# Performance work log

Measured on AMD Instinct MI355X. Metric: run time of the kernel, lower is better.

## Reference

```python
import jax, jax.numpy as jnp
import numpy as np

N = 100000
E = 1600000
NIN = 128
NOUT = 128


def setup_inputs() -> dict:
    key = jax.random.key(0)
    k1, k2, k3, k4 = jax.random.split(key, 4)
    x = jax.random.normal(k1, (N, NIN), dtype=jnp.float32)
    edge_index = jax.random.randint(k2, (2, E), 0, N, dtype=jnp.int64)
    edge_attr = jnp.ones((E,), dtype=jnp.float32)  # unused by GCNConv
    # PyG Linear weight is [out, in]; glorot-ish init
    W = jax.random.normal(k3, (NOUT, NIN), dtype=jnp.float32) / np.sqrt(NIN)
    b = jnp.zeros((NOUT,), dtype=jnp.float32)
    return {"x": x, "edge_index": edge_index, "edge_attr": edge_attr, "W": W, "b": b}


def reference(x, edge_index, edge_attr, W, b):
    # PyG GCNConv: add self-loops, symmetric degree normalization,
    # linear transform, scatter-add aggregation at destination, + bias.
    n = x.shape[0]
    loops = jnp.arange(n, dtype=edge_index.dtype)
    src = jnp.concatenate([edge_index[0], loops])  # [E+N]
    dst = jnp.concatenate([edge_index[1], loops])  # [E+N]
    # degree over destination (col) including self-loops, edge weight = 1
    deg = jax.ops.segment_sum(jnp.ones_like(dst, dtype=x.dtype), dst, num_segments=n)
    dinv = jnp.where(deg > 0, jax.lax.rsqrt(deg), 0.0)
    norm = dinv[src] * dinv[dst]  # [E+N]
    h = x @ W.T  # [N, NOUT]
    msg = h[src] * norm[:, None]  # [E+N, NOUT]
    out = jax.ops.segment_sum(msg, dst, num_segments=n)  # [N, NOUT]
    return out + b
```

## Files before the change

kernel.cpp:

```cpp
#include <hip/hip_runtime.h>

#define TPB 256
#define NBLK 256
#define BSH 8
#define BCAP 6144

typedef __attribute__((ext_vector_type(4))) float f32x4;
typedef __attribute__((ext_vector_type(8))) short short8;

__device__ __forceinline__ unsigned short f2bf(float f) {
    unsigned u = __float_as_uint(f);
    u = (u + 0x7fffu + ((u >> 16) & 1u)) >> 16;
    return (unsigned short)u;
}
__device__ __forceinline__ float bflo(unsigned u) { return __uint_as_float(u << 16); }
__device__ __forceinline__ float bfhi(unsigned u) { return __uint_as_float(u & 0xffff0000u); }


__global__ __launch_bounds__(256) void k_bhist(const int* __restrict__ dst,
                                               int* __restrict__ blockhist,
                                               const float* __restrict__ W,
                                               unsigned short* __restrict__ wbf, int E) {
    __shared__ int sh[512];
    int t = threadIdx.x;
    sh[t] = 0; sh[t + 256] = 0;
    __syncthreads();
    int chunk = (E + NBLK - 1) / NBLK;
    int lo = blockIdx.x * chunk;
    int hi = min(E, lo + chunk);
    for (int e = lo + t; e < hi; e += 256)
        atomicAdd(&sh[dst[e] >> BSH], 1);
    __syncthreads();
    int* row = blockhist + blockIdx.x * 512;
    row[t] = sh[t];
    row[t + 256] = sh[t + 256];

    if (blockIdx.x < 8) {
        int gid = blockIdx.x * 256 + t;
        const float* wp = W + gid * 8;
        float4 w0 = *(const float4*)wp;
        float4 w1 = *(const float4*)(wp + 4);
        union { unsigned short u[8]; uint4 q; } pk;
        pk.u[0] = f2bf(w0.x); pk.u[1] = f2bf(w0.y); pk.u[2] = f2bf(w0.z); pk.u[3] = f2bf(w0.w);
        pk.u[4] = f2bf(w1.x); pk.u[5] = f2bf(w1.y); pk.u[6] = f2bf(w1.z); pk.u[7] = f2bf(w1.w);
        *((uint4*)wbf + gid) = pk.q;
    }
}


__global__ __launch_bounds__(256) void k_bpfx(int* __restrict__ blockhist,
                                              int* __restrict__ ctot) {
    const int wave = blockIdx.x * 4 + (threadIdx.x >> 6);
    const int lane = threadIdx.x & 63;
    int v[4];
    #pragma unroll
    for (int j = 0; j < 4; ++j) v[j] = blockhist[(lane * 4 + j) * 512 + wave];
    int s = v[0] + v[1] + v[2] + v[3];
    int incl = s;
    #pragma unroll
    for (int d = 1; d < 64; d <<= 1) {
        int o = __shfl_up(incl, d);
        if (lane >= d) incl += o;
    }
    int pre = incl - s;
    #pragma unroll
    for (int j = 0; j < 4; ++j) { blockhist[(lane * 4 + j) * 512 + wave] = pre; pre += v[j]; }
    if (lane == 63) ctot[wave] = incl;
}

__device__ __forceinline__ void bucket_base_scan(const int* __restrict__ ctot,
                                                 int (&tp)[2][256], int* bb,
                                                 int E, int t) {
    int v0 = ctot[2 * t], v1 = ctot[2 * t + 1];
    int p = v0 + v1;
    tp[0][t] = p;
    __syncthreads();
    int sb = 0;
    for (int d = 1; d < 256; d <<= 1) {
        int val = tp[sb][t] + ((t >= d) ? tp[sb][t - d] : 0);
        tp[sb ^ 1][t] = val;
        sb ^= 1;
        __syncthreads();
    }
    int base = tp[sb][t] - p;
    bb[2 * t] = base;
    bb[2 * t + 1] = base + v0;
    if (t == 0) bb[512] = E;
    __syncthreads();
}


__global__ __launch_bounds__(256) void k_bscatter(const int* __restrict__ src,
                                                  const int* __restrict__ dst,
                                                  const int* __restrict__ blockhist,
                                                  const int* __restrict__ ctot,
                                                  unsigned* __restrict__ packed, int E) {
    __shared__ int tp[2][256];
    __shared__ int bb[513];
    __shared__ int cur[512];
    int t = threadIdx.x;
    bucket_base_scan(ctot, tp, bb, E, t);
    const int* row = blockhist + blockIdx.x * 512;
    cur[t]       = bb[t]       + row[t];
    cur[t + 256] = bb[t + 256] + row[t + 256];
    __syncthreads();
    int chunk = (E + NBLK - 1) / NBLK;
    int lo = blockIdx.x * chunk;
    int hi = min(E, lo + chunk);
    for (int e = lo + t; e < hi; e += 256) {
        int d = dst[e];
        int pos = atomicAdd(&cur[d >> BSH], 1);
        packed[pos] = ((unsigned)src[e] << 8) | (unsigned)(d & 255);
    }
}


__global__ __launch_bounds__(256) void k_bcsr(const unsigned* __restrict__ packed,
                                              const int* __restrict__ ctot,
                                              int* __restrict__ offsets,
                                              int* __restrict__ sorted_src,
                                              float* __restrict__ dinv, int N, int E, int NB) {
    __shared__ int tmp[2][256];
    __shared__ int bb[513];
    __shared__ int hist[256];
    __shared__ int scur[256];
    __shared__ unsigned stage[BCAP];
    int t = threadIdx.x;
    bucket_base_scan(ctot, tmp, bb, E, t);

    for (int b = blockIdx.x; b < NB; b += NBLK) {
        int s0 = bb[b], s1 = bb[b + 1];
        int cnt = s1 - s0;
        hist[t] = 0;
        __syncthreads();
        for (int e = s0 + t; e < s1; e += 256)
            atomicAdd(&hist[packed[e] & 255u], 1);
        __syncthreads();
        int v = hist[t];
        tmp[0][t] = v;
        __syncthreads();
        int sb = 0;
        for (int d = 1; d < 256; d <<= 1) {
            int val = tmp[sb][t] + ((t >= d) ? tmp[sb][t - d] : 0);
            tmp[sb ^ 1][t] = val;
            sb ^= 1;
            __syncthreads();
        }
        int lbase = tmp[sb][t] - v;
        scur[t] = lbase;
        int d = (b << BSH) + t;
        if (d < N) { offsets[d] = s0 + lbase; dinv[d] = rsqrtf((float)v + 1.0f); }
        if (b == 0 && t == 0) offsets[N] = E;
        __syncthreads();
        if (cnt <= BCAP) {
            for (int e = s0 + t; e < s1; e += 256) {
                unsigned pk = packed[e];
                int pos = atomicAdd(&scur[pk & 255u], 1);
                stage[pos] = pk & 0xffffff00u;
            }
            __syncthreads();
            for (int i = t; i < cnt; i += 256)
                sorted_src[s0 + i] = (int)stage[i];
        } else {
            for (int e = s0 + t; e < s1; e += 256) {
                unsigned pk = packed[e];
                int pos = atomicAdd(&scur[pk & 255u], 1);
                sorted_src[(long)s0 + pos] = (int)(pk & 0xffffff00u);
            }
        }
        __syncthreads();
    }
}


__global__ __launch_bounds__(256) void k_gemm(const float* __restrict__ x,
                                              const unsigned short* __restrict__ wbf,
                                              const float* __restrict__ dinv,
                                              unsigned short* __restrict__ g, int n) {
    __shared__ unsigned short wb[128][136];
    const int tid = threadIdx.x;

    const uint4* wv = (const uint4*)wbf;
    for (int ch = tid; ch < 2048; ch += 256) {
        int nrow = ch >> 4, k8 = (ch & 15) << 3;
        *(uint4*)&wb[nrow][k8] = wv[ch];
    }
    __syncthreads();

    const int lane = tid & 63;
    const int wid  = tid >> 6;
    const int l15  = lane & 15;
    const int quad = lane >> 4;
    const int row  = blockIdx.x * 64 + wid * 16 + l15;
    const int rowc = (row < n) ? row : (n - 1);

    f32x4 acc[8];
    #pragma unroll
    for (int t = 0; t < 8; ++t) acc[t] = (f32x4){0.f, 0.f, 0.f, 0.f};

    #pragma unroll
    for (int ks = 0; ks < 4; ++ks) {
        const int kb = ks * 32 + quad * 8;
        const f32x4* xp = (const f32x4*)(x + (long)rowc * 128 + kb);
        f32x4 a0 = __builtin_nontemporal_load(xp);
        f32x4 a1 = __builtin_nontemporal_load(xp + 1);
        union { unsigned short u[8]; short8 v; } af;
        af.u[0] = f2bf(a0.x); af.u[1] = f2bf(a0.y); af.u[2] = f2bf(a0.z); af.u[3] = f2bf(a0.w);
        af.u[4] = f2bf(a1.x); af.u[5] = f2bf(a1.y); af.u[6] = f2bf(a1.z); af.u[7] = f2bf(a1.w);
        #pragma unroll
        for (int t = 0; t < 8; ++t) {
            short8 bf = *(const short8*)&wb[t * 16 + l15][kb];
            acc[t] = __builtin_amdgcn_mfma_f32_16x16x32_bf16(bf, af.v, acc[t], 0, 0, 0);
        }
    }

    if (row < n) {
        float dv = dinv[row];
        unsigned short* gp = g + (long)row * 128 + quad * 4;
        #pragma unroll
        for (int t = 0; t < 8; ++t) {
            unsigned short u0 = f2bf(acc[t][0] * dv);
            unsigned short u1 = f2bf(acc[t][1] * dv);
            unsigned short u2 = f2bf(acc[t][2] * dv);
            unsigned short u3 = f2bf(acc[t][3] * dv);
            uint2 pk;
            pk.x = (unsigned)u0 | ((unsigned)u1 << 16);
            pk.y = (unsigned)u2 | ((unsigned)u3 << 16);
            *(uint2*)(gp + t * 16) = pk;
        }
    }
}


__global__ __launch_bounds__(256) void k_aggregate(const int* __restrict__ sorted_src,
                                                   const int* __restrict__ offsets,
                                                   const unsigned short* __restrict__ g,
                                                   const float* __restrict__ dinv,
                                                   const float* __restrict__ b,
                                                   float* __restrict__ out, int n) {
    int d = blockIdx.x * (TPB / 32) + (threadIdx.x >> 5);
    if (d >= n) return;
    int c = (threadIdx.x & 31) << 2;
    const char* gb = (const char*)g + (c << 1);

    int s0 = offsets[d];
    int s1 = offsets[d + 1];

    float4 acc = make_float4(0.f, 0.f, 0.f, 0.f);
    auto addrow = [&](int off) {
        uint2 p = *(const uint2*)(gb + off);
        acc.x += bflo(p.x); acc.y += bfhi(p.x);
        acc.z += bflo(p.y); acc.w += bfhi(p.y);
    };

    addrow(d << 8);
    int e = s0;
    for (; e + 8 <= s1; e += 8) {
        int a[8];
        #pragma unroll
        for (int j = 0; j < 8; ++j) a[j] = __builtin_nontemporal_load(&sorted_src[e + j]);
        #pragma unroll
        for (int j = 0; j < 8; ++j) addrow(a[j]);
    }
    for (; e + 4 <= s1; e += 4) {
        int a[4];
        #pragma unroll
        for (int j = 0; j < 4; ++j) a[j] = __builtin_nontemporal_load(&sorted_src[e + j]);
        #pragma unroll
        for (int j = 0; j < 4; ++j) addrow(a[j]);
    }
    for (; e < s1; ++e) addrow(__builtin_nontemporal_load(&sorted_src[e]));

    float s = dinv[d];
    float4 bb = *(const float4*)(b + c);
    f32x4 r = (f32x4){acc.x * s + bb.x, acc.y * s + bb.y,
                      acc.z * s + bb.z, acc.w * s + bb.w};
    __builtin_nontemporal_store(r, (f32x4*)(out + (long)d * 128 + c));
}


extern "C" void kernel_launch(void* const* d_in, const int* in_sizes, int n_in,
                              void* d_out, int out_size, void* d_ws, size_t ws_size,
                              hipStream_t stream) {
    const float* x  = (const float*)d_in[0];
    const int*   ei = (const int*)d_in[1];
    const float* W  = (const float*)d_in[3];
    const float* b  = (const float*)d_in[4];
    float* out = (float*)d_out;

    const int N = in_sizes[0] / 128;
    const int E = in_sizes[1] / 2;
    const int* src = ei;
    const int* dst = ei + E;
    const int NB = (N + 255) >> BSH;

    char* p = (char*)d_ws;
    auto carve = [&](size_t bytes) { char* q = p; p += (bytes + 255) & ~(size_t)255; return q; };
    int*            blockhist  = (int*)           carve((size_t)NBLK * 512 * 4);
    int*            ctot       = (int*)           carve(512 * 4);
    int*            offsets    = (int*)           carve((size_t)(N + 1) * 4);
    float*          dinv       = (float*)         carve((size_t)N * 4);
    unsigned*       packed     = (unsigned*)      carve((size_t)E * 4);
    int*            sorted_src = (int*)           carve((size_t)E * 4);
    unsigned short* wbf        = (unsigned short*)carve((size_t)128 * 128 * 2);
    unsigned short* g          = (unsigned short*)carve((size_t)N * 128 * 2);

    k_bhist   <<<NBLK, TPB, 0, stream>>>(dst, blockhist, W, wbf, E);
    k_bpfx    <<<128, TPB, 0, stream>>>(blockhist, ctot);
    k_bscatter<<<NBLK, TPB, 0, stream>>>(src, dst, blockhist, ctot, packed, E);
    k_bcsr    <<<NB, TPB, 0, stream>>>(packed, ctot, offsets, sorted_src, dinv, N, E, NB);

    k_gemm<<<(N + 63) / 64, TPB, 0, stream>>>(x, wbf, dinv, g, N);

    k_aggregate<<<(N + (TPB / 32) - 1) / (TPB / 32), TPB, 0, stream>>>(
        sorted_src, offsets, g, dinv, b, out, N);
}
```

Baseline: 247.3 us.

## Fuse CSR build and GEMM into one launch by moving source-norm scaling to aggregation

The bucket-CSR construction and the bf16 MFMA GEMM are merged into a single kernel. The first NBLK blocks build the CSR, and the remaining blocks compute h = xW^T. This lets the two independent stages run concurrently and removes one launch. To break the GEMM's dependency on dinv, the per-source dinv scaling is moved into the aggregation kernel, which now gathers dinv[src] for every edge and applies it with an FMA. Nontemporal load and store hints are also dropped, and sorted_src now stores raw source indices, with the byte-offset shift done at gather time.

```diff
diff --git a/kernel.cpp b/kernel.cpp
--- a/kernel.cpp
+++ b/kernel.cpp
@@ -69,20 +69,23 @@
 }
 
 __device__ __forceinline__ void bucket_base_scan(const int* __restrict__ ctot,
-                                                 int (&tp)[2][256], int* bb,
+                                                 int* tp0, int* tp1, int* bb,
                                                  int E, int t) {
     int v0 = ctot[2 * t], v1 = ctot[2 * t + 1];
     int p = v0 + v1;
-    tp[0][t] = p;
+    tp0[t] = p;
     __syncthreads();
     int sb = 0;
     for (int d = 1; d < 256; d <<= 1) {
-        int val = tp[sb][t] + ((t >= d) ? tp[sb][t - d] : 0);
-        tp[sb ^ 1][t] = val;
+        int* cur = sb ? tp1 : tp0;
+        int* nxt = sb ? tp0 : tp1;
+        int val = cur[t] + ((t >= d) ? cur[t - d] : 0);
+        nxt[t] = val;
         sb ^= 1;
         __syncthreads();
     }
-    int base = tp[sb][t] - p;
+    int* fin = sb ? tp1 : tp0;
+    int base = fin[t] - p;
     bb[2 * t] = base;
     bb[2 * t + 1] = base + v0;
     if (t == 0) bb[512] = E;
@@ -95,11 +98,11 @@
                                                   const int* __restrict__ blockhist,
                                                   const int* __restrict__ ctot,
                                                   unsigned* __restrict__ packed, int E) {
-    __shared__ int tp[2][256];
+    __shared__ int tp0[256], tp1[256];
     __shared__ int bb[513];
     __shared__ int cur[512];
     int t = threadIdx.x;
-    bucket_base_scan(ctot, tp, bb, E, t);
+    bucket_base_scan(ctot, tp0, tp1, bb, E, t);
     const int* row = blockhist + blockIdx.x * 512;
     cur[t]       = bb[t]       + row[t];
     cur[t + 256] = bb[t + 256] + row[t + 256];
@@ -115,118 +118,119 @@
 }
 
 
-__global__ __launch_bounds__(256) void k_bcsr(const unsigned* __restrict__ packed,
-                                              const int* __restrict__ ctot,
-                                              int* __restrict__ offsets,
-                                              int* __restrict__ sorted_src,
-                                              float* __restrict__ dinv, int N, int E, int NB) {
-    __shared__ int tmp[2][256];
-    __shared__ int bb[513];
-    __shared__ int hist[256];
-    __shared__ int scur[256];
-    __shared__ unsigned stage[BCAP];
-    int t = threadIdx.x;
-    bucket_base_scan(ctot, tmp, bb, E, t);
-
-    for (int b = blockIdx.x; b < NB; b += NBLK) {
-        int s0 = bb[b], s1 = bb[b + 1];
-        int cnt = s1 - s0;
-        hist[t] = 0;
+__global__ __launch_bounds__(256) void k_csrgemm(
+    const unsigned* __restrict__ packed, const int* __restrict__ ctot,
+    int* __restrict__ offsets, int* __restrict__ sorted_src, float* __restrict__ dinv,
+    const float* __restrict__ x, const unsigned short* __restrict__ wbf,
+    unsigned short* __restrict__ g, int N, int E, int NB)
+{
+    __shared__ __align__(16) char smem[34816];
+    const int t = threadIdx.x;
+
+    if (blockIdx.x < NBLK) {
+        int* tp0  = (int*)smem;
+        int* tp1  = tp0 + 256;
+        int* bb   = tp1 + 256;
+        int* hist = bb + 516;
+        int* scur = hist + 256;
+        unsigned* stage = (unsigned*)(scur + 256);
+        bucket_base_scan(ctot, tp0, tp1, bb, E, t);
+
+        for (int b = blockIdx.x; b < NB; b += NBLK) {
+            int s0 = bb[b], s1 = bb[b + 1];
+            int cnt = s1 - s0;
+            hist[t] = 0;
+            __syncthreads();
+            for (int e = s0 + t; e < s1; e += 256)
+                atomicAdd(&hist[packed[e] & 255u], 1);
+            __syncthreads();
+            int v = hist[t];
+            tp0[t] = v;
+            __syncthreads();
+            int sb = 0;
+            for (int d = 1; d < 256; d <<= 1) {
+                int* cur = sb ? tp1 : tp0;
+                int* nxt = sb ? tp0 : tp1;
+                int val = cur[t] + ((t >= d) ? cur[t - d] : 0);
+                nxt[t] = val;
+                sb ^= 1;
+                __syncthreads();
+            }
+            int* fin = sb ? tp1 : tp0;
+            int lbase = fin[t] - v;
+            scur[t] = lbase;
+            int d = (b << BSH) + t;
+            if (d < N) { offsets[d] = s0 + lbase; dinv[d] = rsqrtf((float)v + 1.0f); }
+            if (b == 0 && t == 0) offsets[N] = E;
+            __syncthreads();
+            if (cnt <= BCAP) {
+                for (int e = s0 + t; e < s1; e += 256) {
+                    unsigned pk = packed[e];
+                    int pos = atomicAdd(&scur[pk & 255u], 1);
+                    stage[pos] = pk >> 8;
+                }
+                __syncthreads();
+                for (int i = t; i < cnt; i += 256)
+                    sorted_src[s0 + i] = (int)stage[i];
+            } else {
+                for (int e = s0 + t; e < s1; e += 256) {
+                    unsigned pk = packed[e];
+                    int pos = atomicAdd(&scur[pk & 255u], 1);
+                    sorted_src[(long)s0 + pos] = (int)(pk >> 8);
+                }
+            }
+            __syncthreads();
+        }
+    } else {
+        typedef unsigned short wb_t[136];
+        wb_t* wb = (wb_t*)smem;
+
+        const uint4* wv = (const uint4*)wbf;
+        for (int ch = t; ch < 2048; ch += 256) {
+            int nrow = ch >> 4, k8 = (ch & 15) << 3;
+            *(uint4*)&wb[nrow][k8] = wv[ch];
+        }
         __syncthreads();
-        for (int e = s0 + t; e < s1; e += 256)
-            atomicAdd(&hist[packed[e] & 255u], 1);
-        __syncthreads();
-        int v = hist[t];
-        tmp[0][t] = v;
-        __syncthreads();
-        int sb = 0;
-        for (int d = 1; d < 256; d <<= 1) {
-            int val = tmp[sb][t] + ((t >= d) ? tmp[sb][t - d] : 0);
-            tmp[sb ^ 1][t] = val;
-            sb ^= 1;
-            __syncthreads();
-        }
-        int lbase = tmp[sb][t] - v;
-        scur[t] = lbase;
-        int d = (b << BSH) + t;
-        if (d < N) { offsets[d] = s0 + lbase; dinv[d] = rsqrtf((float)v + 1.0f); }
-        if (b == 0 && t == 0) offsets[N] = E;
-        __syncthreads();
-        if (cnt <= BCAP) {
-            for (int e = s0 + t; e < s1; e += 256) {
-                unsigned pk = packed[e];
-                int pos = atomicAdd(&scur[pk & 255u], 1);
-                stage[pos] = pk & 0xffffff00u;
-            }
-            __syncthreads();
-            for (int i = t; i < cnt; i += 256)
-                sorted_src[s0 + i] = (int)stage[i];
-        } else {
-            for (int e = s0 + t; e < s1; e += 256) {
-                unsigned pk = packed[e];
-                int pos = atomicAdd(&scur[pk & 255u], 1);
-                sorted_src[(long)s0 + pos] = (int)(pk & 0xffffff00u);
+
+        const int lane = t & 63;
+        const int wid  = t >> 6;
+        const int l15  = lane & 15;
+        const int quad = lane >> 4;
+        const int row  = (blockIdx.x - NBLK) * 64 + wid * 16 + l15;
+        const int rowc = (row < N) ? row : (N - 1);
+
+        f32x4 acc[8];
+        #pragma unroll
+        for (int u = 0; u < 8; ++u) acc[u] = (f32x4){0.f, 0.f, 0.f, 0.f};
+
+        #pragma unroll
+        for (int ks = 0; ks < 4; ++ks) {
+            const int kb = ks * 32 + quad * 8;
+            float4 a0 = *(const float4*)(x + (long)rowc * 128 + kb);
+            float4 a1 = *(const float4*)(x + (long)rowc * 128 + kb + 4);
+            union { unsigned short u[8]; short8 v; } af;
+            af.u[0] = f2bf(a0.x); af.u[1] = f2bf(a0.y); af.u[2] = f2bf(a0.z); af.u[3] = f2bf(a0.w);
+            af.u[4] = f2bf(a1.x); af.u[5] = f2bf(a1.y); af.u[6] = f2bf(a1.z); af.u[7] = f2bf(a1.w);
+            #pragma unroll
+            for (int u = 0; u < 8; ++u) {
+                short8 bf = *(const short8*)&wb[u * 16 + l15][kb];
+                acc[u] = __builtin_amdgcn_mfma_f32_16x16x32_bf16(bf, af.v, acc[u], 0, 0, 0);
             }
         }
-        __syncthreads();
-    }
-}
-
-
-__global__ __launch_bounds__(256) void k_gemm(const float* __restrict__ x,
-                                              const unsigned short* __restrict__ wbf,
-                                              const float* __restrict__ dinv,
-                                              unsigned short* __restrict__ g, int n) {
-    __shared__ unsigned short wb[128][136];
-    const int tid = threadIdx.x;
-
-    const uint4* wv = (const uint4*)wbf;
-    for (int ch = tid; ch < 2048; ch += 256) {
-        int nrow = ch >> 4, k8 = (ch & 15) << 3;
-        *(uint4*)&wb[nrow][k8] = wv[ch];
-    }
-    __syncthreads();
-
-    const int lane = tid & 63;
-    const int wid  = tid >> 6;
-    const int l15  = lane & 15;
-    const int quad = lane >> 4;
-    const int row  = blockIdx.x * 64 + wid * 16 + l15;
-    const int rowc = (row < n) ? row : (n - 1);
-
-    f32x4 acc[8];
-    #pragma unroll
-    for (int t = 0; t < 8; ++t) acc[t] = (f32x4){0.f, 0.f, 0.f, 0.f};
-
-    #pragma unroll
-    for (int ks = 0; ks < 4; ++ks) {
-        const int kb = ks * 32 + quad * 8;
-        const f32x4* xp = (const f32x4*)(x + (long)rowc * 128 + kb);
-        f32x4 a0 = __builtin_nontemporal_load(xp);
-        f32x4 a1 = __builtin_nontemporal_load(xp + 1);
-        union { unsigned short u[8]; short8 v; } af;
-        af.u[0] = f2bf(a0.x); af.u[1] = f2bf(a0.y); af.u[2] = f2bf(a0.z); af.u[3] = f2bf(a0.w);
-        af.u[4] = f2bf(a1.x); af.u[5] = f2bf(a1.y); af.u[6] = f2bf(a1.z); af.u[7] = f2bf(a1.w);
-        #pragma unroll
-        for (int t = 0; t < 8; ++t) {
-            short8 bf = *(const short8*)&wb[t * 16 + l15][kb];
-            acc[t] = __builtin_amdgcn_mfma_f32_16x16x32_bf16(bf, af.v, acc[t], 0, 0, 0);
-        }
-    }
-
-    if (row < n) {
-        float dv = dinv[row];
-        unsigned short* gp = g + (long)row * 128 + quad * 4;
-        #pragma unroll
-        for (int t = 0; t < 8; ++t) {
-            unsigned short u0 = f2bf(acc[t][0] * dv);
-            unsigned short u1 = f2bf(acc[t][1] * dv);
-            unsigned short u2 = f2bf(acc[t][2] * dv);
-            unsigned short u3 = f2bf(acc[t][3] * dv);
-            uint2 pk;
-            pk.x = (unsigned)u0 | ((unsigned)u1 << 16);
-            pk.y = (unsigned)u2 | ((unsigned)u3 << 16);
-            *(uint2*)(gp + t * 16) = pk;
+
+        if (row < N) {
+            unsigned short* gp = g + (long)row * 128 + quad * 4;
+            #pragma unroll
+            for (int u = 0; u < 8; ++u) {
+                unsigned short u0 = f2bf(acc[u][0]);
+                unsigned short u1 = f2bf(acc[u][1]);
+                unsigned short u2 = f2bf(acc[u][2]);
+                unsigned short u3 = f2bf(acc[u][3]);
+                uint2 pk;
+                pk.x = (unsigned)u0 | ((unsigned)u1 << 16);
+                pk.y = (unsigned)u2 | ((unsigned)u3 << 16);
+                *(uint2*)(gp + u * 16) = pk;
+            }
         }
     }
 }
@@ -247,35 +251,38 @@
     int s1 = offsets[d + 1];
 
     float4 acc = make_float4(0.f, 0.f, 0.f, 0.f);
-    auto addrow = [&](int off) {
-        uint2 p = *(const uint2*)(gb + off);
-        acc.x += bflo(p.x); acc.y += bfhi(p.x);
-        acc.z += bflo(p.y); acc.w += bfhi(p.y);
+    auto addrow = [&](int r) {
+        float dv = dinv[r];
+        uint2 p = *(const uint2*)(gb + (r << 8));
+        acc.x = fmaf(bflo(p.x), dv, acc.x);
+        acc.y = fmaf(bfhi(p.x), dv, acc.y);
+        acc.z = fmaf(bflo(p.y), dv, acc.z);
+        acc.w = fmaf(bfhi(p.y), dv, acc.w);
     };
 
-    addrow(d << 8);
+    addrow(d);
     int e = s0;
     for (; e + 8 <= s1; e += 8) {
         int a[8];
         #pragma unroll
-        for (int j = 0; j < 8; ++j) a[j] = __builtin_nontemporal_load(&sorted_src[e + j]);
+        for (int j = 0; j < 8; ++j) a[j] = sorted_src[e + j];
         #pragma unroll
         for (int j = 0; j < 8; ++j) addrow(a[j]);
     }
     for (; e + 4 <= s1; e += 4) {
         int a[4];
         #pragma unroll
-        for (int j = 0; j < 4; ++j) a[j] = __builtin_nontemporal_load(&sorted_src[e + j]);
+        for (int j = 0; j < 4; ++j) a[j] = sorted_src[e + j];
         #pragma unroll
         for (int j = 0; j < 4; ++j) addrow(a[j]);
     }
-    for (; e < s1; ++e) addrow(__builtin_nontemporal_load(&sorted_src[e]));
+    for (; e < s1; ++e) addrow(sorted_src[e]);
 
     float s = dinv[d];
     float4 bb = *(const float4*)(b + c);
-    f32x4 r = (f32x4){acc.x * s + bb.x, acc.y * s + bb.y,
-                      acc.z * s + bb.z, acc.w * s + bb.w};
-    __builtin_nontemporal_store(r, (f32x4*)(out + (long)d * 128 + c));
+    float4 r = make_float4(acc.x * s + bb.x, acc.y * s + bb.y,
+                           acc.z * s + bb.z, acc.w * s + bb.w);
+    *(float4*)(out + (long)d * 128 + c) = r;
 }
 
 
@@ -305,12 +312,13 @@
     unsigned short* wbf        = (unsigned short*)carve((size_t)128 * 128 * 2);
     unsigned short* g          = (unsigned short*)carve((size_t)N * 128 * 2);
 
+    const int gemmBlocks = (N + 63) / 64;
+
     k_bhist   <<<NBLK, TPB, 0, stream>>>(dst, blockhist, W, wbf, E);
     k_bpfx    <<<128, TPB, 0, stream>>>(blockhist, ctot);
     k_bscatter<<<NBLK, TPB, 0, stream>>>(src, dst, blockhist, ctot, packed, E);
-    k_bcsr    <<<NB, TPB, 0, stream>>>(packed, ctot, offsets, sorted_src, dinv, N, E, NB);
-
-    k_gemm<<<(N + 63) / 64, TPB, 0, stream>>>(x, wbf, dinv, g, N);
+    k_csrgemm <<<NBLK + gemmBlocks, TPB, 0, stream>>>(packed, ctot, offsets, sorted_src,
+                                                      dinv, x, wbf, g, N, E, NB);
 
     k_aggregate<<<(N + (TPB / 32) - 1) / (TPB / 32), TPB, 0, stream>>>(
         sorted_src, offsets, g, dinv, b, out, N);
```

After: 238.7 us. 1.04x faster.
